# Kernel optimization log

Hardware: AMD Instinct MI355X
Metric: run time of the kernel (lower is better)

Reference implementation:

```python
import jax, jax.numpy as jnp
import numpy as np

N_NODES = 100_000
N_EDGES = 3_200_000
NUM_FEATURES = 128
HIDDEN = 128
NUM_CLASSES = 10
LAYERS = 3
NUM_GRAPHS = 256
EPS = 1e-5


def setup_inputs() -> dict:
    key = jax.random.key(0)
    ks = jax.random.split(key, 12)
    s = 0.05
    x = jax.random.normal(ks[0], (N_NODES, NUM_FEATURES), jnp.float32)
    edge_index = jax.random.randint(ks[1], (2, N_EDGES), 0, N_NODES, dtype=jnp.int32)
    batch = jnp.sort(jax.random.randint(ks[2], (N_NODES,), 0, NUM_GRAPHS, dtype=jnp.int32))
    lin1_W = jax.random.normal(ks[3], (NUM_FEATURES, HIDDEN), jnp.float32) * s
    lin1_b = jnp.zeros((HIDDEN,), jnp.float32)
    conv_W = jax.random.normal(ks[4], (LAYERS, HIDDEN, HIDDEN), jnp.float32) * s
    conv_b = jnp.zeros((LAYERS, HIDDEN), jnp.float32)
    mlp_W1 = jax.random.normal(ks[5], (HIDDEN, HIDDEN), jnp.float32) * s
    mlp_b1 = jnp.zeros((HIDDEN,), jnp.float32)
    mlp_W2 = jax.random.normal(ks[6], (HIDDEN, NUM_CLASSES), jnp.float32) * s
    mlp_b2 = jnp.zeros((NUM_CLASSES,), jnp.float32)
    return {
        'x': x, 'edge_index': edge_index, 'batch': batch,
        'lin1_W': lin1_W, 'lin1_b': lin1_b,
        'conv_W': conv_W, 'conv_b': conv_b,
        'mlp_W1': mlp_W1, 'mlp_b1': mlp_b1,
        'mlp_W2': mlp_W2, 'mlp_b2': mlp_b2,
    }


def reference(x, edge_index, batch, lin1_W, lin1_b, conv_W, conv_b,
              mlp_W1, mlp_b1, mlp_W2, mlp_b2):
    N = x.shape[0]
    # GCN with self-loops, all-ones edge_weight, symmetric normalization.
    loop = jnp.arange(N, dtype=edge_index.dtype)
    src = jnp.concatenate([edge_index[0], loop])
    dst = jnp.concatenate([edge_index[1], loop])
    ew = jnp.ones(src.shape[0], x.dtype)
    deg = jax.ops.segment_sum(ew, dst, num_segments=N)
    dinv = jnp.where(deg > 0, jax.lax.rsqrt(deg), 0.0)
    norm = dinv[src] * dinv[dst]  # [E+N]

    h = jax.nn.relu(x @ lin1_W + lin1_b)  # dropout is identity at eval
    for i in range(conv_W.shape[0]):
        hw = h @ conv_W[i]                       # [N,H]
        msg = hw[src] * norm[:, None]            # [E+N,H] gather
        h = jax.ops.segment_sum(msg, dst, num_segments=N) + conv_b[i]
        h = jax.nn.relu(h)
        # full-tensor LayerNorm (normalized_shape == x.size(), no affine)
        mu = jnp.mean(h)
        var = jnp.mean(jnp.square(h - mu))
        h = (h - mu) * jax.lax.rsqrt(var + EPS)

    # global mean pooling over graphs
    cnt = jax.ops.segment_sum(jnp.ones((N,), x.dtype), batch, num_segments=NUM_GRAPHS)
    pooled = jax.ops.segment_sum(h, batch, num_segments=NUM_GRAPHS) / jnp.maximum(cnt, 1.0)[:, None]

    g = jax.nn.relu(pooled @ mlp_W1 + mlp_b1)
    scores = g @ mlp_W2 + mlp_b2
    return jax.nn.log_softmax(scores, axis=-1)
```

## Files before the change

kernel.cpp:

```cpp
#include <hip/hip_runtime.h>
#include <math.h>

#define NN 100000
#define HH 128
#define NCLS 10
#define NGRAPH 256
#define EPSLN 1e-5f
#define NB 196
#define NBLK 256
#define NREP 8

typedef __attribute__((ext_vector_type(8))) short short8;
typedef __attribute__((ext_vector_type(4))) float f32x4;

static __device__ __forceinline__ unsigned short f2bf(float f){
  unsigned u = __float_as_uint(f);
  u = u + 0x7fffu + ((u >> 16) & 1u);
  return (unsigned short)(u >> 16);
}
static __device__ __forceinline__ float bf2f(unsigned short h){
  return __uint_as_float(((unsigned)h) << 16);
}

__global__ __launch_bounds__(1024) void bucket_hist(
    const int* __restrict__ dst, int E,
    int* __restrict__ gbucket, int* __restrict__ blkbase)
{
  __shared__ int lh[NREP*NB];
  int tid = threadIdx.x;
  for (int i = tid; i < NREP*NB; i += 1024) lh[i] = 0;
  __syncthreads();
  int rep = (tid >> 7) & (NREP-1);
  int* lhr = &lh[rep*NB];
  int per = (E + gridDim.x - 1) / gridDim.x;
  int s = blockIdx.x * per, e = min(E, s + per);
  for (int j = s + tid; j < e; j += 1024)
    atomicAdd(&lhr[dst[j] >> 9], 1);
  __syncthreads();
  for (int i = tid; i < NREP*NB; i += 1024){
    int r = i / NB, bkt = i - r*NB;
    blkbase[((size_t)blockIdx.x*NREP + r)*NB + bkt] = atomicAdd(&gbucket[bkt], lh[i]);
  }
}

__global__ __launch_bounds__(256) void misc_prep(
    const int* __restrict__ gbucket, int* __restrict__ bucket_base, int E,
    int* __restrict__ row_ptr, int N,
    float* __restrict__ params, float* __restrict__ stats, int* __restrict__ counters,
    const float* __restrict__ lin1W, const float* __restrict__ convW,
    unsigned short* __restrict__ WtAll, float* __restrict__ csums)
{
  int b = blockIdx.x;
  if (b == 0){
    if (threadIdx.x == 0){
      int run = 0;
      for (int i = 0; i < NB; i++){ bucket_base[i] = run; run += gbucket[i]; }
      bucket_base[NB] = run;
      row_ptr[N] = E;
      params[0] = 0.f;
      params[1] = 1.f;
      for (int i = 0; i < 6; i++) stats[i] = 0.f;
      for (int i = 0; i < 3; i++) counters[i] = 0;
    }
  } else if (b <= 3){
    int m = b - 1;
    if (threadIdx.x < HH){
      const float* w = convW + (size_t)m*HH*HH;
      float s = 0.f;
      for (int k = 0; k < HH; k++) s += w[k*HH + threadIdx.x];
      csums[m*HH + threadIdx.x] = s;
    }
  } else {
    int m = b - 4;
    const float* srcW = (m == 0) ? lin1W : convW + (size_t)(m-1)*HH*HH;
    unsigned short* dstW = WtAll + (size_t)m*HH*HH;
    for (int i = threadIdx.x; i < HH*HH; i += 256){
      int k = i >> 7, nn2 = i & 127;
      dstW[nn2*HH + k] = f2bf(srcW[i]);
    }
  }
}

__global__ __launch_bounds__(1024) void bucket_scatter(
    const int* __restrict__ src, const int* __restrict__ dst, int E,
    const int* __restrict__ bucket_base, const int* __restrict__ blkbase,
    unsigned* __restrict__ ebuf)
{
  __shared__ int lcur[NREP*NB];
  int tid = threadIdx.x;
  for (int i = tid; i < NREP*NB; i += 1024){
    int r = i / NB, bkt = i - r*NB;
    lcur[i] = bucket_base[bkt] + blkbase[((size_t)blockIdx.x*NREP + r)*NB + bkt];
  }
  __syncthreads();
  int rep = (tid >> 7) & (NREP-1);
  int* lcr = &lcur[rep*NB];
  int per = (E + gridDim.x - 1) / gridDim.x;
  int s = blockIdx.x * per, e = min(E, s + per);
  for (int j = s + tid; j < e; j += 1024){
    int d = dst[j];
    int p = atomicAdd(&lcr[d >> 9], 1);
    ebuf[p] = (((unsigned)(d & 511)) << 23) | (unsigned)src[j];
  }
}

__global__ __launch_bounds__(1024) void bucket_fill(
    const unsigned* __restrict__ ebuf,
    const int* __restrict__ bucket_base, int N,
    int* __restrict__ row_ptr, float* __restrict__ dinv,
    int* __restrict__ csr)
{
  __shared__ int ldeg[512];
  __shared__ int lscan[512];
  __shared__ int lcur[512];
  int b = blockIdx.x, tid = threadIdx.x;
  int node0 = b << 9;
  int nn = min(512, N - node0);
  for (int i = tid; i < 512; i += 1024) ldeg[i] = 0;
  __syncthreads();
  int s = bucket_base[b], e = bucket_base[b + 1];
  for (int j = s + tid; j < e; j += 1024)
    atomicAdd(&ldeg[ebuf[j] >> 23], 1);
  __syncthreads();
  if (tid < 512) lscan[tid] = ldeg[tid];
  __syncthreads();
  for (int off = 1; off < 512; off <<= 1){
    int v = (tid < 512 && tid >= off) ? lscan[tid - off] : 0;
    __syncthreads();
    if (tid < 512) lscan[tid] += v;
    __syncthreads();
  }
  if (tid < nn){
    int rp = s + lscan[tid] - ldeg[tid];
    row_ptr[node0 + tid] = rp;
    lcur[tid] = rp;
    dinv[node0 + tid] = rsqrtf((float)(ldeg[tid] + 1));
  }
  __syncthreads();
  for (int j = s + tid; j < e; j += 1024){
    unsigned pk = ebuf[j];
    int p = atomicAdd(&lcur[pk >> 23], 1);
    csr[p] = (int)(pk & 0x7fffffu);
  }
}

__global__ __launch_bounds__(256) void gemm_mfma(
    const float* __restrict__ A32, const unsigned short* __restrict__ A16,
    const unsigned short* __restrict__ Wt,
    const float* __restrict__ bias, const float* __restrict__ dinv,
    const float* __restrict__ params, const float* __restrict__ colsum,
    unsigned short* __restrict__ out, int n, int mode)
{
  __shared__ unsigned short As[128*128];
  __shared__ unsigned short Ws[128*128];
  int tid = threadIdx.x;
  int rb = blockIdx.x * 128;

  #pragma unroll
  for (int rep = 0; rep < 8; rep++){
    int idx = rep*256 + tid;
    int r = idx >> 4, j = idx & 15;
    uint4 v = *(const uint4*)&Wt[r*HH + j*8];
    *(uint4*)&Ws[r*128 + ((j ^ (r & 7)) << 3)] = v;
  }
  if (mode == 1){
    #pragma unroll
    for (int rep = 0; rep < 8; rep++){
      int idx = rep*256 + tid;
      int r = idx >> 4, j = idx & 15;
      int row = rb + r;
      uint4 v = make_uint4(0,0,0,0);
      if (row < n) v = *(const uint4*)&A16[(size_t)row*HH + j*8];
      *(uint4*)&As[r*128 + ((j ^ (r & 7)) << 3)] = v;
    }
  } else {
    #pragma unroll
    for (int rep = 0; rep < 16; rep++){
      int idx = rep*256 + tid;
      int r = idx >> 5, j4 = idx & 31;
      int row = rb + r;
      float4 v = make_float4(0,0,0,0);
      if (row < n) v = *(const float4*)&A32[(size_t)row*HH + j4*4];
      uint2 pk;
      pk.x = (unsigned)f2bf(v.x) | ((unsigned)f2bf(v.y) << 16);
      pk.y = (unsigned)f2bf(v.z) | ((unsigned)f2bf(v.w) << 16);
      int uidx = r*128 + ((((j4 >> 1) ^ (r & 7)) << 3)) + (j4 & 1)*4;
      *(uint2*)&As[uidx] = pk;
    }
  }
  __syncthreads();

  int l = tid & 63, w = tid >> 6;
  int lr = l & 15, lk = l >> 4;
  f32x4 acc[2][8];
  #pragma unroll
  for (int mt = 0; mt < 2; mt++)
    #pragma unroll
    for (int nt = 0; nt < 8; nt++) acc[mt][nt] = (f32x4)(0.f);

  #pragma unroll
  for (int kc = 0; kc < 4; kc++){
    short8 af[2];
    #pragma unroll
    for (int mt = 0; mt < 2; mt++){
      int row = w*32 + mt*16 + lr;
      af[mt] = *(const short8*)&As[row*128 + (((kc*4 + lk) ^ (row & 7)) << 3)];
    }
    #pragma unroll
    for (int nt = 0; nt < 8; nt++){
      int col = nt*16 + lr;
      short8 bf = *(const short8*)&Ws[col*128 + (((kc*4 + lk) ^ (col & 7)) << 3)];
      acc[0][nt] = __builtin_amdgcn_mfma_f32_16x16x32_bf16(af[0], bf, acc[0][nt], 0, 0, 0);
      acc[1][nt] = __builtin_amdgcn_mfma_f32_16x16x32_bf16(af[1], bf, acc[1][nt], 0, 0, 0);
    }
  }

  float mu = 0.f, rsig = 1.f;
  if (mode == 1){ mu = params[0]; rsig = params[1]; }
  float dvs[2][4];
  #pragma unroll
  for (int mt = 0; mt < 2; mt++)
    #pragma unroll
    for (int r = 0; r < 4; r++){
      int row = rb + w*32 + mt*16 + lk*4 + r;
      dvs[mt][r] = (mode == 1 && row < n) ? dinv[row] : 0.f;
    }
  #pragma unroll
  for (int nt = 0; nt < 8; nt++){
    int col = nt*16 + lr;
    float cs = (mode == 1) ? colsum[col] : 0.f;
    float bb = (mode == 0) ? bias[col] : 0.f;
    #pragma unroll
    for (int mt = 0; mt < 2; mt++){
      #pragma unroll
      for (int r = 0; r < 4; r++){
        int row = rb + w*32 + mt*16 + lk*4 + r;
        if (row < n){
          float a = acc[mt][nt][r];
          float vv = (mode == 0) ? fmaxf(a + bb, 0.f)
                                 : dvs[mt][r] * rsig * (a - mu*cs);
          out[(size_t)row*HH + col] = f2bf(vv);
        }
      }
    }
  }
}

__global__ __launch_bounds__(256) void aggregate(
    const unsigned* __restrict__ hw, const int* __restrict__ row_ptr,
    const int* __restrict__ csr, const float* __restrict__ dinv,
    const float* __restrict__ bias, unsigned* __restrict__ hout,
    float2* __restrict__ partials, int n)
{
  int wid = __builtin_amdgcn_readfirstlane(threadIdx.x >> 6);
  int node = blockIdx.x * 4 + wid;
  if (node >= n) return;
  int half = blockIdx.y;
  int l = threadIdx.x & 63;
  int sub = l >> 5;
  int f = l & 31;
  int base = half*32 + f;

  float ax = 0.f, ay = 0.f;
  if (sub == 0){
    unsigned sv = hw[node*64 + base];
    ax = __uint_as_float(sv << 16);
    ay = __uint_as_float(sv & 0xffff0000u);
  }
  int s0 = row_ptr[node], s1 = row_ptr[node+1];
  int j = s0;
  for (; j + 16 <= s1; j += 16){
    int idx[8];
    #pragma unroll
    for (int u = 0; u < 8; u++){
      int a0 = csr[j + 2*u];
      int a1 = csr[j + 2*u + 1];
      idx[u] = sub ? a1 : a0;
    }
    unsigned v[8];
    #pragma unroll
    for (int u = 0; u < 8; u++) v[u] = hw[idx[u]*64 + base];
    #pragma unroll
    for (int u = 0; u < 8; u++){
      ax += __uint_as_float(v[u] << 16);
      ay += __uint_as_float(v[u] & 0xffff0000u);
    }
  }
  for (; j + 2 <= s1; j += 2){
    int a0 = csr[j], a1 = csr[j + 1];
    unsigned v = hw[(sub ? a1 : a0)*64 + base];
    ax += __uint_as_float(v << 16);
    ay += __uint_as_float(v & 0xffff0000u);
  }
  if (j < s1 && sub == 0){
    unsigned v = hw[csr[j]*64 + base];
    ax += __uint_as_float(v << 16);
    ay += __uint_as_float(v & 0xffff0000u);
  }
  ax += __shfl_xor(ax, 32, 64);
  ay += __shfl_xor(ay, 32, 64);

  float dv = dinv[node];
  float2 bb = ((const float2*)bias)[base];
  float rx = fmaxf(fmaf(dv, ax, bb.x), 0.f);
  float ry = fmaxf(fmaf(dv, ay, bb.y), 0.f);
  if (sub == 0)
    hout[node*64 + base] = (unsigned)f2bf(rx) | ((unsigned)f2bf(ry) << 16);

  float s = rx + ry, q = rx*rx + ry*ry;
  #pragma unroll
  for (int off = 16; off > 0; off >>= 1){
    s += __shfl_xor(s, off, 64);
    q += __shfl_xor(q, off, 64);
  }
  if (l == 0) partials[node*2 + half] = make_float2(s, q);
}

__global__ __launch_bounds__(256) void finalize_ln(
    const float2* __restrict__ partials, int n2, float* __restrict__ stats,
    int* __restrict__ counter, float* __restrict__ params)
{
  int tid = threadIdx.x;
  float s = 0.f, q = 0.f;
  for (int i = blockIdx.x*256 + tid; i < n2; i += gridDim.x*256){
    float2 p = partials[i];
    s += p.x; q += p.y;
  }
  #pragma unroll
  for (int off = 32; off > 0; off >>= 1){
    s += __shfl_xor(s, off, 64);
    q += __shfl_xor(q, off, 64);
  }
  __shared__ float ssm[4], qsm[4];
  int wave = tid >> 6, lane = tid & 63;
  if (lane == 0){ ssm[wave] = s; qsm[wave] = q; }
  __syncthreads();
  if (tid == 0){
    atomicAdd(&stats[0], ssm[0]+ssm[1]+ssm[2]+ssm[3]);
    atomicAdd(&stats[1], qsm[0]+qsm[1]+qsm[2]+qsm[3]);
    __threadfence();
    int done = atomicAdd(counter, 1);
    if (done == (int)gridDim.x - 1){
      float S = atomicAdd(&stats[0], 0.f);
      float Q = atomicAdd(&stats[1], 0.f);
      const float inv = 1.f / ((float)NN * (float)HH);
      float mu = S * inv;
      float var = Q * inv - mu*mu;
      params[0] = mu;
      params[1] = rsqrtf(var + EPSLN);
    }
  }
}

__global__ __launch_bounds__(1024) void pool_mlp(
    const unsigned* __restrict__ h, const int* __restrict__ batch,
    const float* __restrict__ params, const float* __restrict__ W1,
    const float* __restrict__ b1, const float* __restrict__ W2,
    const float* __restrict__ b2, float* __restrict__ out, int n)
{
  __shared__ float W1s[128*128];
  __shared__ float2 psum[16][64];
  __shared__ float pooled[128];
  __shared__ float gact[128];
  __shared__ float sc[16];
  __shared__ int se[2];
  int g = blockIdx.x, tid = threadIdx.x;

  #pragma unroll
  for (int rep = 0; rep < 4; rep++){
    int i = rep*1024 + tid;
    *(float4*)&W1s[i*4] = *(const float4*)&W1[i*4];
  }
  if (tid < 2){
    int v = g + tid;
    int lo = 0, hi = n;
    while (lo < hi){ int mid = (lo+hi) >> 1; if (batch[mid] < v) lo = mid+1; else hi = mid; }
    se[tid] = lo;
  }
  __syncthreads();
  int start = se[0], end = se[1];
  int w = tid >> 6, l = tid & 63;
  float sx = 0.f, sy = 0.f;
  for (int v = start + w; v < end; v += 16){
    unsigned u = h[v*64 + l];
    sx += __uint_as_float(u << 16);
    sy += __uint_as_float(u & 0xffff0000u);
  }
  psum[w][l] = make_float2(sx, sy);
  __syncthreads();
  if (tid < 64){
    float ax = 0.f, ay = 0.f;
    #pragma unroll
    for (int ww = 0; ww < 16; ww++){
      float2 p = psum[ww][tid];
      ax += p.x; ay += p.y;
    }
    float cnt = (float)((end - start) > 0 ? (end - start) : 1);
    float mu = params[0], rs = params[1];
    pooled[tid*2]   = rs * (ax / cnt - mu);
    pooled[tid*2+1] = rs * (ay / cnt - mu);
  }
  __syncthreads();
  if (tid < 128){
    float a = b1[tid];
    for (int k = 0; k < HH; k++) a = fmaf(pooled[k], W1s[k*HH + tid], a);
    gact[tid] = fmaxf(a, 0.f);
  }
  __syncthreads();
  if (tid < NCLS){
    float s = b2[tid];
    for (int k = 0; k < HH; k++) s = fmaf(gact[k], W2[k*NCLS + tid], s);
    sc[tid] = s;
  }
  __syncthreads();
  if (tid == 0){
    float m = sc[0];
    for (int j = 1; j < NCLS; j++) m = fmaxf(m, sc[j]);
    float lse = 0.f;
    for (int j = 0; j < NCLS; j++) lse += expf(sc[j] - m);
    lse = logf(lse);
    for (int j = 0; j < NCLS; j++) out[g*NCLS + j] = sc[j] - m - lse;
  }
}

extern "C" void kernel_launch(void* const* d_in, const int* in_sizes, int n_in,
                              void* d_out, int out_size, void* d_ws, size_t ws_size,
                              hipStream_t stream)
{
  const float* x      = (const float*)d_in[0];
  const int*   ei     = (const int*)d_in[1];
  const int*   batch  = (const int*)d_in[2];
  const float* lin1_W = (const float*)d_in[3];
  const float* lin1_b = (const float*)d_in[4];
  const float* conv_W = (const float*)d_in[5];
  const float* conv_b = (const float*)d_in[6];
  const float* mlp_W1 = (const float*)d_in[7];
  const float* mlp_b1 = (const float*)d_in[8];
  const float* mlp_W2 = (const float*)d_in[9];
  const float* mlp_b2 = (const float*)d_in[10];

  const int N = in_sizes[2];
  const int E = in_sizes[1] / 2;

  char* ws = (char*)d_ws;
  size_t off = 0;
  auto alloc = [&](size_t bytes)->char*{
    char* p = ws + off; off += (bytes + 255) & ~(size_t)255; return p;
  };
  unsigned short* bufA = (unsigned short*)alloc((size_t)N*HH*2);
  unsigned short* bufB = (unsigned short*)alloc((size_t)N*HH*2);
  unsigned short* WtAll= (unsigned short*)alloc((size_t)4*HH*HH*2);
  int*      csr     = (int*)     alloc((size_t)E*4);
  unsigned* ebuf    = (unsigned*)alloc((size_t)E*4);
  int*      row_ptr = (int*)     alloc((size_t)(N+1)*4);
  float*    dinv    = (float*)   alloc((size_t)N*4);
  int*      gbucket = (int*)     alloc((size_t)NB*4);
  int*      bucket_base = (int*) alloc((size_t)(NB+1)*4);
  int*      blkbase = (int*)     alloc((size_t)NBLK*NREP*NB*4);
  float*    params  = (float*)   alloc(256);
  float*    stats   = (float*)   alloc(256);
  int*      counters= (int*)     alloc(256);
  float*    csums   = (float*)   alloc(3*HH*4);
  float2*   partials= (float2*)  alloc((size_t)N*2*8);

  const int* srcp = ei;
  const int* dstp = ei + E;

  hipMemsetAsync(gbucket, 0, (size_t)NB*4, stream);
  bucket_hist<<<NBLK, 1024, 0, stream>>>(dstp, E, gbucket, blkbase);
  misc_prep<<<8, 256, 0, stream>>>(gbucket, bucket_base, E, row_ptr, N,
                                   params, stats, counters,
                                   lin1_W, conv_W, WtAll, csums);
  bucket_scatter<<<NBLK, 1024, 0, stream>>>(srcp, dstp, E, bucket_base, blkbase, ebuf);
  bucket_fill<<<NB, 1024, 0, stream>>>(ebuf, bucket_base, N, row_ptr, dinv, csr);

  int gblocks = (N + 127) / 128;
  gemm_mfma<<<gblocks, 256, 0, stream>>>(x, nullptr, WtAll, lin1_b,
                                         nullptr, nullptr, nullptr, bufA, N, 0);
  dim3 agrid((N + 3) / 4, 2);
  for (int i = 0; i < 3; i++){
    gemm_mfma<<<gblocks, 256, 0, stream>>>(nullptr, bufA, WtAll + (size_t)(i+1)*HH*HH,
                                           nullptr, dinv, params + 2*i, csums + i*HH,
                                           bufB, N, 1);
    aggregate<<<agrid, 256, 0, stream>>>((const unsigned*)bufB, row_ptr, csr, dinv,
                                         conv_b + i*HH, (unsigned*)bufA, partials, N);
    finalize_ln<<<64, 256, 0, stream>>>(partials, 2*N, stats + 2*i,
                                        counters + i, params + 2*(i+1));
  }
  pool_mlp<<<NGRAPH, 1024, 0, stream>>>((const unsigned*)bufA, batch, params + 6,
                                        mlp_W1, mlp_b1, mlp_W2, mlp_b2,
                                        (float*)d_out, N);
}
```

Before: 649.2 us.

## Slice hidden features into 16-wide column planes so aggregation gathers stay cache-resident

The transform GEMM now writes its output in a slice-major layout: 8 planes of 16 bf16 features per node. The aggregate kernel runs a flat grid ordered slice by slice, so each group of blocks gathers from one 3.2 MB plane that can stay in L2/LLC instead of spilling across the whole 25 MB feature matrix. Each wave splits into 8 lanes per edge times 8 edges in parallel, with vectorized int4 CSR index loads after an alignment prologue. The trade-offs: each gather fetches only 32 bytes per neighbor, the LayerNorm partials buffer grows fourfold, and more cross-lane shuffles are needed for the reduction.

```diff
diff --git a/kernel.cpp b/kernel.cpp
--- a/kernel.cpp
+++ b/kernel.cpp
@@ -20,6 +20,12 @@
 }
 static __device__ __forceinline__ float bf2f(unsigned short h){
   return __uint_as_float(((unsigned)h) << 16);
+}
+static __device__ __forceinline__ float bfx(unsigned v){
+  return __uint_as_float(v << 16);
+}
+static __device__ __forceinline__ float bfy(unsigned v){
+  return __uint_as_float(v & 0xffff0000u);
 }
 
 __global__ __launch_bounds__(1024) void bucket_hist(
@@ -237,9 +243,12 @@
         int row = rb + w*32 + mt*16 + lk*4 + r;
         if (row < n){
           float a = acc[mt][nt][r];
-          float vv = (mode == 0) ? fmaxf(a + bb, 0.f)
-                                 : dvs[mt][r] * rsig * (a - mu*cs);
-          out[(size_t)row*HH + col] = f2bf(vv);
+          if (mode == 0){
+            out[(size_t)row*HH + col] = f2bf(fmaxf(a + bb, 0.f));
+          } else {
+            float vv = dvs[mt][r] * rsig * (a - mu*cs);
+            out[((size_t)nt*n + row)*16 + lr] = f2bf(vv);
+          }
         }
       }
     }
@@ -250,70 +259,80 @@
     const unsigned* __restrict__ hw, const int* __restrict__ row_ptr,
     const int* __restrict__ csr, const float* __restrict__ dinv,
     const float* __restrict__ bias, unsigned* __restrict__ hout,
-    float2* __restrict__ partials, int n)
-{
+    float2* __restrict__ partials, int n, int nb4)
+{
+  int bx = blockIdx.x;
+  int slice = bx / nb4;
+  int nblk  = bx - slice*nb4;
   int wid = __builtin_amdgcn_readfirstlane(threadIdx.x >> 6);
-  int node = blockIdx.x * 4 + wid;
+  int node = nblk*4 + wid;
   if (node >= n) return;
-  int half = blockIdx.y;
   int l = threadIdx.x & 63;
-  int sub = l >> 5;
-  int f = l & 31;
-  int base = half*32 + f;
+  int e = l >> 3;
+  int f = l & 7;
+  unsigned sb = (unsigned)slice * (unsigned)n;
 
   float ax = 0.f, ay = 0.f;
-  if (sub == 0){
-    unsigned sv = hw[node*64 + base];
-    ax = __uint_as_float(sv << 16);
-    ay = __uint_as_float(sv & 0xffff0000u);
+  if (e == 0){
+    unsigned sv = hw[(size_t)(sb + node)*8 + f];
+    ax = bfx(sv); ay = bfy(sv);
   }
   int s0 = row_ptr[node], s1 = row_ptr[node+1];
   int j = s0;
+  int jal = (s0 + 3) & ~3;
+  if (jal > s1) jal = s1;
+  int pre = jal - j;
+  if (e < pre){
+    unsigned v = hw[(size_t)(sb + csr[j + e])*8 + f];
+    ax += bfx(v); ay += bfy(v);
+  }
+  j = jal;
+  #define SEL4(q) ((e3==0)?(q).x:(e3==1)?(q).y:(e3==2)?(q).z:(q).w)
   for (; j + 16 <= s1; j += 16){
-    int idx[8];
-    #pragma unroll
-    for (int u = 0; u < 8; u++){
-      int a0 = csr[j + 2*u];
-      int a1 = csr[j + 2*u + 1];
-      idx[u] = sub ? a1 : a0;
-    }
-    unsigned v[8];
-    #pragma unroll
-    for (int u = 0; u < 8; u++) v[u] = hw[idx[u]*64 + base];
-    #pragma unroll
-    for (int u = 0; u < 8; u++){
-      ax += __uint_as_float(v[u] << 16);
-      ay += __uint_as_float(v[u] & 0xffff0000u);
-    }
-  }
-  for (; j + 2 <= s1; j += 2){
-    int a0 = csr[j], a1 = csr[j + 1];
-    unsigned v = hw[(sub ? a1 : a0)*64 + base];
-    ax += __uint_as_float(v << 16);
-    ay += __uint_as_float(v & 0xffff0000u);
-  }
-  if (j < s1 && sub == 0){
-    unsigned v = hw[csr[j]*64 + base];
-    ax += __uint_as_float(v << 16);
-    ay += __uint_as_float(v & 0xffff0000u);
-  }
-  ax += __shfl_xor(ax, 32, 64);
-  ay += __shfl_xor(ay, 32, 64);
+    int4 q0 = *(const int4*)&csr[j];
+    int4 q1 = *(const int4*)&csr[j+4];
+    int4 q2 = *(const int4*)&csr[j+8];
+    int4 q3 = *(const int4*)&csr[j+12];
+    int e3 = e & 3;
+    int a0 = SEL4(q0), a1 = SEL4(q1), b0 = SEL4(q2), b1 = SEL4(q3);
+    int idA = (e < 4) ? a0 : a1;
+    int idB = (e < 4) ? b0 : b1;
+    unsigned vA = hw[(size_t)(sb + idA)*8 + f];
+    unsigned vB = hw[(size_t)(sb + idB)*8 + f];
+    ax += bfx(vA) + bfx(vB);
+    ay += bfy(vA) + bfy(vB);
+  }
+  for (; j + 8 <= s1; j += 8){
+    int4 q0 = *(const int4*)&csr[j];
+    int4 q1 = *(const int4*)&csr[j+4];
+    int e3 = e & 3;
+    int a0 = SEL4(q0), a1 = SEL4(q1);
+    int idA = (e < 4) ? a0 : a1;
+    unsigned v = hw[(size_t)(sb + idA)*8 + f];
+    ax += bfx(v); ay += bfy(v);
+  }
+  #undef SEL4
+  int rem = s1 - j;
+  if (e < rem){
+    unsigned v = hw[(size_t)(sb + csr[j + e])*8 + f];
+    ax += bfx(v); ay += bfy(v);
+  }
+  ax += __shfl_xor(ax, 8, 64); ax += __shfl_xor(ax, 16, 64); ax += __shfl_xor(ax, 32, 64);
+  ay += __shfl_xor(ay, 8, 64); ay += __shfl_xor(ay, 16, 64); ay += __shfl_xor(ay, 32, 64);
 
   float dv = dinv[node];
-  float2 bb = ((const float2*)bias)[base];
+  float2 bb = ((const float2*)bias)[slice*8 + f];
   float rx = fmaxf(fmaf(dv, ax, bb.x), 0.f);
   float ry = fmaxf(fmaf(dv, ay, bb.y), 0.f);
-  if (sub == 0)
-    hout[node*64 + base] = (unsigned)f2bf(rx) | ((unsigned)f2bf(ry) << 16);
 
   float s = rx + ry, q = rx*rx + ry*ry;
-  #pragma unroll
-  for (int off = 16; off > 0; off >>= 1){
-    s += __shfl_xor(s, off, 64);
-    q += __shfl_xor(q, off, 64);
-  }
-  if (l == 0) partials[node*2 + half] = make_float2(s, q);
+  s += __shfl_xor(s, 1, 64); s += __shfl_xor(s, 2, 64); s += __shfl_xor(s, 4, 64);
+  q += __shfl_xor(q, 1, 64); q += __shfl_xor(q, 2, 64); q += __shfl_xor(q, 4, 64);
+
+  if (e == 0){
+    hout[(size_t)node*64 + slice*8 + f] = (unsigned)f2bf(rx) | ((unsigned)f2bf(ry) << 16);
+    if (f == 0) partials[(size_t)slice*n + node] = make_float2(s, q);
+  }
 }
 
 __global__ __launch_bounds__(256) void finalize_ln(
@@ -461,7 +480,7 @@
   float*    stats   = (float*)   alloc(256);
   int*      counters= (int*)     alloc(256);
   float*    csums   = (float*)   alloc(3*HH*4);
-  float2*   partials= (float2*)  alloc((size_t)N*2*8);
+  float2*   partials= (float2*)  alloc((size_t)N*8*sizeof(float2));
 
   const int* srcp = ei;
   const int* dstp = ei + E;
@@ -477,14 +496,15 @@
   int gblocks = (N + 127) / 128;
   gemm_mfma<<<gblocks, 256, 0, stream>>>(x, nullptr, WtAll, lin1_b,
                                          nullptr, nullptr, nullptr, bufA, N, 0);
-  dim3 agrid((N + 3) / 4, 2);
+  int nb4 = (N + 3) / 4;
   for (int i = 0; i < 3; i++){
     gemm_mfma<<<gblocks, 256, 0, stream>>>(nullptr, bufA, WtAll + (size_t)(i+1)*HH*HH,
                                            nullptr, dinv, params + 2*i, csums + i*HH,
                                            bufB, N, 1);
-    aggregate<<<agrid, 256, 0, stream>>>((const unsigned*)bufB, row_ptr, csr, dinv,
-                                         conv_b + i*HH, (unsigned*)bufA, partials, N);
-    finalize_ln<<<64, 256, 0, stream>>>(partials, 2*N, stats + 2*i,
+    aggregate<<<8*nb4, 256, 0, stream>>>((const unsigned*)bufB, row_ptr, csr, dinv,
+                                         conv_b + i*HH, (unsigned*)bufA,
+                                         partials, N, nb4);
+    finalize_ln<<<64, 256, 0, stream>>>(partials, 8*N, stats + 2*i,
                                         counters + i, params + 2*(i+1));
   }
   pool_mlp<<<NGRAPH, 1024, 0, stream>>>((const unsigned*)bufA, batch, params + 6,
```

Result: slower. 1.407 ms (+116.7%).
